# Kernel tuning notes

Measured on AMD Instinct MI355X. Metric: run time of the kernel, lower is better.

Reference implementation:

```python
import jax, jax.numpy as jnp
import numpy as np
from jax import lax

VDECAY, VTH, GRAD_WIN, GRAD_AMP = 0.5, 0.5, 0.5, 1.0

@jax.custom_vjp
def spike(v):
    return (v > VTH).astype(v.dtype)

def _spike_fwd(v):
    return spike(v), v

def _spike_bwd(v, g):
    # rectangular surrogate gradient
    win = (jnp.abs(v - VTH) <= GRAD_WIN).astype(g.dtype)
    return (GRAD_AMP * g * win,)

spike.defvjp(_spike_fwd, _spike_bwd)

def setup_inputs() -> dict:
    key = jax.random.key(0)
    ks = jax.random.split(key, 3)
    B, D_IN, T, H, D_OUT = 256, 700, 250, 1024, 20
    spike_data = (jax.random.uniform(ks[0], (B, D_IN, T)) < 0.1).astype(jnp.float32)
    W_hid = jax.random.normal(ks[1], (H, D_IN), dtype=jnp.float32) * (1.0 / np.sqrt(D_IN))
    W_out = jax.random.normal(ks[2], (D_OUT, H), dtype=jnp.float32) * (1.0 / np.sqrt(H))
    return {
        "spike_data": spike_data,
        "W_hid": W_hid,
        "W_out": W_out,
        "hid_spike0": jnp.zeros((B, H), jnp.float32),
        "hid_volt0": jnp.zeros((B, H), jnp.float32),
        "out_spike0": jnp.zeros((B, D_OUT), jnp.float32),
        "out_volt0": jnp.zeros((B, D_OUT), jnp.float32),
        "batch_size": 256,
        "spike_ts": 250,
    }

def reference(spike_data, W_hid, W_out, hid_spike0, hid_volt0, out_spike0, out_volt0, batch_size, spike_ts):
    # [B, D_in, T] -> [T, B, D_in] for scan over time
    xs = jnp.moveaxis(spike_data.reshape(batch_size, -1, spike_ts), -1, 0)

    def step(carry, s_in):
        hs, hv, os_, ov = carry
        hv = hv * VDECAY * (1.0 - hs) + s_in @ W_hid.T      # leaky integrate, reset on spike
        hs = spike(hv)                                       # hidden spikes
        ov = ov * VDECAY * (1.0 - os_) + hs @ W_out.T
        os_ = spike(ov)
        return (hs, hv, os_, ov), os_

    _, out_spikes = lax.scan(step, (hid_spike0, hid_volt0, out_spike0, out_volt0), xs)
    return jnp.sum(out_spikes, axis=0)  # [B, D_out] spike counts
```

## Files before the change

kernel.cpp:

```cpp
#include <hip/hip_runtime.h>
#include <stdint.h>

#define B      256
#define DIN    700
#define T      250
#define H      1024
#define DOUT   20
#define NW_IN  11
#define NW_INP 12
#define NW_H   16
#define LMAX   160
#define JSENT2 22512

typedef unsigned long long u64;

__global__ void prep_weights(const float* __restrict__ W_hid,
                             const float* __restrict__ W_out,
                             float* __restrict__ Wt,
                             float* __restrict__ WoT) {
    int idx = blockIdx.x * 256 + threadIdx.x;
    if (blockIdx.x < 2800) {
        int d = idx / H;
        int h = idx - d * H;
        Wt[idx] = W_hid[h * DIN + d];
    } else {
        int i = idx - 2800 * 256;
        int h = i / DOUT;
        int o = i - h * DOUT;
        WoT[i] = W_out[o * H + h];
    }
}

__global__ void prep_bits(const float* __restrict__ spk,
                          u64* __restrict__ bits) {
    int b  = blockIdx.x >> 2;
    int wc = blockIdx.x & 3;
    int t  = threadIdx.x;
    if (t >= T) return;
    int w0 = wc * 3;
    int w1 = (wc == 3) ? NW_IN : w0 + 3;
    const float* base = spk + (size_t)b * DIN * T + t;
    for (int w = w0; w < w1; ++w) {
        u64 m = 0;
#pragma unroll
        for (int j = 0; j < 64; ++j) {
            int d = (w << 6) + j;
            if (d < DIN) {
                float x = base[(size_t)d * T];
                m |= (u64)(x > 0.5f) << j;
            }
        }
        bits[((size_t)b * T + t) * NW_INP + w] = m;
    }
}

__global__ void __launch_bounds__(256)
prep_lists2(const u64* __restrict__ bits,
            unsigned short* __restrict__ lists,
            unsigned* __restrict__ nrow) {
    __shared__ unsigned short scr[4][LMAX];

    int wv   = threadIdx.x >> 6;
    int lane = threadIdx.x & 63;
    int row  = blockIdx.x * 4 + wv;

    const u64* wp = bits + (size_t)row * NW_INP;
    u64 mw = (lane < NW_IN) ? wp[lane] : 0ull;

    for (int i = lane; i < LMAX; i += 64) scr[wv][i] = (unsigned short)JSENT2;

    u64 lowmask = (1ull << lane) - 1ull;
    int pos = 0;
    unsigned counts = 0;

#pragma unroll
    for (int p = 0; p < 4; ++p) {
        int jlo = 175 * p, jhi = jlo + 175;
        int n = 0;
        for (int k = jlo >> 6; k <= (jhi - 1) >> 6; ++k) {
            u64 m = __shfl(mw, k);
            int lo = jlo - (k << 6);
            int hi = jhi - (k << 6);
            if (lo > 0)  m &= ~((1ull << lo) - 1ull);
            if (hi < 64) m &= (1ull << hi) - 1ull;
            if ((m >> lane) & 1ull) {
                int q = pos + n + __popcll(m & lowmask);
                int jl = (k << 6) + lane - jlo;
                if (q < LMAX)
                    scr[wv][q] = (unsigned short)(jl * 128 + ((jl & 7) << 4));
            }
            n += __popcll(m);
        }
        int c = (n + 3) >> 2;
        counts |= (unsigned)c << (8 * p);
        pos += c * 4;
    }

    if (lane == 0) nrow[row] = counts;
    __syncthreads();

    const unsigned* s32 = (const unsigned*)scr[wv];
    unsigned* g32 = (unsigned*)(lists + (size_t)row * LMAX);
    g32[lane] = s32[lane];
    if (lane < 16) g32[64 + lane] = s32[64 + lane];
}

__global__ void __launch_bounds__(256)
sort_rows(const unsigned* __restrict__ nrow,
          unsigned char* __restrict__ perm) {
    __shared__ int cnt[8][32];
    __shared__ int off[8][32];
    int b = blockIdx.x, tid = threadIdx.x;
    cnt[tid >> 5][tid & 31] = 0;
    __syncthreads();
    unsigned cc = 0; int half = 0, lt = 0;
    if (tid < T) {
        cc = nrow[b * T + tid];
        half = tid >= 125;
        lt = tid - half * 125;
#pragma unroll
        for (int p = 0; p < 4; ++p) {
            int c = (cc >> (8 * p)) & 0xff; if (c > 31) c = 31;
            atomicAdd(&cnt[p * 2 + half][c], 1);
        }
    }
    __syncthreads();
    if (tid < 8) {
        int s = 0;
        for (int i = 0; i < 32; ++i) { off[tid][i] = s; s += cnt[tid][i]; cnt[tid][i] = 0; }
    }
    __syncthreads();
    if (tid < T) {
#pragma unroll
        for (int p = 0; p < 4; ++p) {
            int c = (cc >> (8 * p)) & 0xff; if (c > 31) c = 31;
            int sidx = p * 2 + half;
            int rank = off[sidx][c] + atomicAdd(&cnt[sidx][c], 1);
            perm[((size_t)b * 8 + sidx) * 128 + rank] = (unsigned char)lt;
        }
    }
}

__global__ void __launch_bounds__(512, 8)
hidden_slice3(const unsigned short* __restrict__ lists,
              const unsigned* __restrict__ nrow,
              const unsigned char* __restrict__ perm,
              const float* __restrict__ Wt,
              const float* __restrict__ hs0,
              const float* __restrict__ hv0,
              u64* __restrict__ hsbits) {
    __shared__ float wlds[176 * 32];
    __shared__ float cur[125 * 32];

    int s    = blockIdx.x;
    int b    = blockIdx.y;
    int tid  = threadIdx.x;
    int wv   = tid >> 6;
    int lane = tid & 63;
    int g    = lane >> 3;
    int li   = lane & 7;
    int lxor = li << 4;
    int l    = lane & 31;

    float keep = 0.0f;
    if (wv == 0) {
        int h = s * 32 + l;
        keep = hv0[b * H + h] * 0.5f * (1.0f - hs0[b * H + h]);
    }
    unsigned* hp = (unsigned*)hsbits;

    for (int th = 0; th < 2; ++th) {
        for (int p = 0; p < 4; ++p) {
            {
                int jr  = tid >> 3;
                int lis = tid & 7;
#pragma unroll
                for (int bj = 0; bj < 192; bj += 64) {
                    int jl = bj + jr;
                    if (jl < 176) {
                        float4 v = make_float4(0.0f, 0.0f, 0.0f, 0.0f);
                        if (jl < 175)
                            v = *(const float4*)(Wt + (size_t)(p * 175 + jl) * H + s * 32 + lis * 4);
                        *(float4*)((char*)wlds + jl * 128 + ((lis ^ (jl & 7)) << 4)) = v;
                    }
                }
            }
            __syncthreads();

            const unsigned char* pm = perm + ((size_t)b * 8 + p * 2 + th) * 128;

#pragma unroll
            for (int sweep = 0; sweep < 2; ++sweep) {
                int rr = sweep * 64 + wv * 8 + g;
                if (rr < 125) {
                    int lr  = pm[rr];
                    int r   = th * 125 + lr;
                    int row = b * T + r;
                    unsigned cc = nrow[row];
                    int c = (cc >> (8 * p)) & 0xff;
                    int offc = 0;
                    if (p > 0) offc += (cc & 0xff);
                    if (p > 1) offc += ((cc >> 8) & 0xff);
                    if (p > 2) offc += ((cc >> 16) & 0xff);
                    const uint2* qp = (const uint2*)(lists + (size_t)row * LMAX + offc * 4);
                    char* cp = (char*)cur + lr * 128 + ((li ^ (lr & 7)) << 4);

                    float a0, a1, a2, a3;
                    if (p == 0) {
                        a0 = a1 = a2 = a3 = 0.0f;
                    } else {
                        float4 cv = *(const float4*)cp;
                        a0 = cv.x; a1 = cv.y; a2 = cv.z; a3 = cv.w;
                    }

                    if (c > 0) {
                        uint2 w2 = qp[0];
                        int ch = 0;
                        for (;;) {
                            uint2 nw = (ch + 1 < c) ? qp[ch + 1] : w2;
                            int e0 = w2.x & 0xffff, e1 = w2.x >> 16;
                            int e2 = w2.y & 0xffff, e3 = w2.y >> 16;
                            float4 v0 = *(const float4*)((char*)wlds + (e0 ^ lxor));
                            float4 v1 = *(const float4*)((char*)wlds + (e1 ^ lxor));
                            float4 v2 = *(const float4*)((char*)wlds + (e2 ^ lxor));
                            float4 v3 = *(const float4*)((char*)wlds + (e3 ^ lxor));
                            a0 += v0.x; a1 += v0.y; a2 += v0.z; a3 += v0.w;
                            a0 += v1.x; a1 += v1.y; a2 += v1.z; a3 += v1.w;
                            a0 += v2.x; a1 += v2.y; a2 += v2.z; a3 += v2.w;
                            a0 += v3.x; a1 += v3.y; a2 += v3.z; a3 += v3.w;
                            ++ch;
                            if (ch >= c) break;
                            w2 = nw;
                        }
                    }
                    float4 o; o.x = a0; o.y = a1; o.z = a2; o.w = a3;
                    *(float4*)cp = o;
                }
            }
            __syncthreads();
        }

        if (wv == 0) {
            for (int lt = 0; lt < 125; ++lt) {
                float cv = *(const float*)((char*)cur + lt * 128 +
                                           (((l >> 2) ^ (lt & 7)) << 4) + (l & 3) * 4);
                float hv = keep + cv;
                bool sp = hv > 0.5f;
                keep = sp ? 0.0f : hv * 0.5f;
                u64 ball = __ballot(sp);
                int t = th * 125 + lt;
                if (lane == 0)
                    hp[(size_t)(b * T + t) * 32 + s] = (unsigned)ball;
            }
        }
        __syncthreads();
    }
}

__global__ void __launch_bounds__(1024)
hidden_fused(const u64* __restrict__ bits,
             const float* __restrict__ Wt,
             const float* __restrict__ hs0,
             const float* __restrict__ hv0,
             u64* __restrict__ hsbits) {
    __shared__ int idx_l[2][256];

    int b = blockIdx.x;
    int h = threadIdx.x;
    int wv   = h >> 6;
    int lane = h & 63;

    float keep = hv0[b * H + h] * 0.5f * (1.0f - hs0[b * H + h]);

    const u64* bb = bits + (size_t)b * T * NW_INP;

    for (int t = 0; t < T; ++t) {
        const u64* wp = bb + (size_t)t * NW_INP;
        u64 w[NW_IN];
#pragma unroll
        for (int k = 0; k < NW_IN; ++k) w[k] = wp[k];

        int base[NW_IN + 1];
        base[0] = 0;
#pragma unroll
        for (int k = 0; k < NW_IN; ++k) base[k + 1] = base[k] + __popcll(w[k]);
        int n = base[NW_IN];

        int buf = t & 1;
        if (wv < NW_IN) {
            u64 m = w[wv];
            if ((m >> lane) & 1ull) {
                int pos = base[wv] + __popcll(m & ((1ull << lane) - 1ull));
                idx_l[buf][pos] = (wv << 6) + lane;
            }
        }
        __syncthreads();

        const int* il = idx_l[buf];
        float cur2 = 0.0f;
        int i = 0;
        for (; i + 8 <= n; i += 8) {
            int j0 = il[i + 0], j1 = il[i + 1], j2 = il[i + 2], j3 = il[i + 3];
            int j4 = il[i + 4], j5 = il[i + 5], j6 = il[i + 6], j7 = il[i + 7];
            float v0 = Wt[(size_t)j0 * H + h];
            float v1 = Wt[(size_t)j1 * H + h];
            float v2 = Wt[(size_t)j2 * H + h];
            float v3 = Wt[(size_t)j3 * H + h];
            float v4 = Wt[(size_t)j4 * H + h];
            float v5 = Wt[(size_t)j5 * H + h];
            float v6 = Wt[(size_t)j6 * H + h];
            float v7 = Wt[(size_t)j7 * H + h];
            cur2 += v0; cur2 += v1; cur2 += v2; cur2 += v3;
            cur2 += v4; cur2 += v5; cur2 += v6; cur2 += v7;
        }
        for (; i < n; ++i) cur2 += Wt[(size_t)il[i] * H + h];

        float hv = keep + cur2;
        bool sp = hv > 0.5f;
        keep = sp ? 0.0f : hv * 0.5f;
        u64 ball = __ballot(sp);
        if (lane == 0)
            hsbits[((size_t)b * T + t) * NW_H + wv] = ball;
    }
}

__global__ void __launch_bounds__(256)
out_currents(const u64* __restrict__ hsbits,
             const float* __restrict__ WoT,
             float* __restrict__ Iout) {
    __shared__ int lidx[4][2][256];

    int wv   = threadIdx.x >> 6;
    int lane = threadIdx.x & 63;
    int row  = blockIdx.x * 4 + wv;

    const u64* wp = hsbits + (size_t)row * NW_H;

    float acc = 0.0f;
#pragma unroll
    for (int g = 0; g < 4; ++g) {
        u64 w[4];
#pragma unroll
        for (int k = 0; k < 4; ++k) w[k] = wp[g * 4 + k];

        int base[5];
        base[0] = 0;
#pragma unroll
        for (int k = 0; k < 4; ++k) base[k + 1] = base[k] + __popcll(w[k]);
        int n = base[4];

        int buf = g & 1;
#pragma unroll
        for (int k = 0; k < 4; ++k) {
            u64 m = w[k];
            if ((m >> lane) & 1ull) {
                int pos = base[k] + __popcll(m & ((1ull << lane) - 1ull));
                lidx[wv][buf][pos] = ((g * 4 + k) << 6) + lane;
            }
        }
        __syncthreads();

        const int* il = lidx[wv][buf];
        int i = 0;
        for (; i + 4 <= n; i += 4) {
            int j0 = il[i + 0], j1 = il[i + 1], j2 = il[i + 2], j3 = il[i + 3];
            if (lane < DOUT) {
                float v0 = WoT[(size_t)j0 * DOUT + lane];
                float v1 = WoT[(size_t)j1 * DOUT + lane];
                float v2 = WoT[(size_t)j2 * DOUT + lane];
                float v3 = WoT[(size_t)j3 * DOUT + lane];
                acc += v0; acc += v1; acc += v2; acc += v3;
            }
        }
        for (; i < n; ++i) {
            if (lane < DOUT) acc += WoT[(size_t)il[i] * DOUT + lane];
        }
    }
    if (lane < DOUT) Iout[(size_t)row * DOUT + lane] = acc;
}

__global__ void __launch_bounds__(256)
out_scan(const float* __restrict__ Iout,
         const float* __restrict__ os0,
         const float* __restrict__ ov0,
         float* __restrict__ outp) {
    __shared__ float pan[T * DOUT];

    int b   = blockIdx.x;
    int tid = threadIdx.x;

    const float* src = Iout + (size_t)b * T * DOUT;
#pragma unroll
    for (int k = 0; k < 20; ++k) {
        int i = k * 256 + tid;
        if (i < T * DOUT) pan[i] = src[i];
    }
    __syncthreads();

    if (tid < DOUT) {
        int o = tid;
        int idx = b * DOUT + o;
        float ov = ov0[idx];
        float os = os0[idx];
        float keep = ov * 0.5f * (1.0f - os);
        float cnt = 0.0f;
#pragma unroll 5
        for (int t = 0; t < T; ++t) {
            float v = keep + pan[t * DOUT + o];
            float sp = (v > 0.5f) ? 1.0f : 0.0f;
            cnt += sp;
            keep = v * 0.5f * (1.0f - sp);
        }
        outp[idx] = cnt;
    }
}

extern "C" void kernel_launch(void* const* d_in, const int* in_sizes, int n_in,
                              void* d_out, int out_size, void* d_ws, size_t ws_size,
                              hipStream_t stream) {
    const float* spike = (const float*)d_in[0];
    const float* W_hid = (const float*)d_in[1];
    const float* W_out = (const float*)d_in[2];
    const float* hs0   = (const float*)d_in[3];
    const float* hv0   = (const float*)d_in[4];
    const float* os0   = (const float*)d_in[5];
    const float* ov0   = (const float*)d_in[6];
    float* outp = (float*)d_out;

    char* ws = (char*)d_ws;
    float*          Wt     = (float*)(ws);
    float*          WoT    = (float*)(ws + 2867200);
    u64*            bits   = (u64*)  (ws + 2949120);
    u64*            hsbits = (u64*)  (ws + 9093120);
    float*          Iout   = (float*)(ws + 17285120);
    unsigned short* lists  = (unsigned short*)(ws + 22405120);
    unsigned*       nrow   = (unsigned*)(ws + 42885120);
    unsigned char*  perm   = (unsigned char*)(ws + 43141120);
    const size_t need = 43403264;

    prep_weights<<<2880, 256, 0, stream>>>(W_hid, W_out, Wt, WoT);
    prep_bits<<<1024, 256, 0, stream>>>(spike, bits);

    if (ws_size >= need) {
        prep_lists2<<<16000, 256, 0, stream>>>(bits, lists, nrow);
        sort_rows<<<B, 256, 0, stream>>>(nrow, perm);
        hidden_slice3<<<dim3(32, 256), 512, 0, stream>>>(lists, nrow, perm, Wt, hs0, hv0, hsbits);
    } else {
        hidden_fused<<<B, 1024, 0, stream>>>(bits, Wt, hs0, hv0, hsbits);
    }

    out_currents<<<16000, 256, 0, stream>>>(hsbits, WoT, Iout);
    out_scan<<<B, 256, 0, stream>>>(Iout, os0, ov0, outp);
}
```

Baseline: 988.0 us.

## Stage W_out^T in LDS and pack three rows per wave in out_currents

The output-current kernel now copies the whole transposed output weight matrix (80 KB) into shared memory once per block. Each wave then handles three (batch, time) rows at once, using 60 of its 64 lanes, and walks the set bits of the hidden spike mask with ctz instead of building index lists in LDS. This removes the per-row list compaction, the barriers and the global gathers, and uses more lanes per wave. In exchange each block must fill 80 KB of LDS, which limits occupancy. Lanes in a wave loop different numbers of times, so they diverge.

```diff
diff --git a/kernel.cpp b/kernel.cpp
--- a/kernel.cpp
+++ b/kernel.cpp
@@ -324,59 +324,46 @@
     }
 }
 
-__global__ void __launch_bounds__(256)
-out_currents(const u64* __restrict__ hsbits,
-             const float* __restrict__ WoT,
-             float* __restrict__ Iout) {
-    __shared__ int lidx[4][2][256];
-
-    int wv   = threadIdx.x >> 6;
-    int lane = threadIdx.x & 63;
-    int row  = blockIdx.x * 4 + wv;
+__global__ void __launch_bounds__(512)
+out_currents2(const u64* __restrict__ hsbits,
+              const float* __restrict__ WoT,
+              float* __restrict__ Iout) {
+    __shared__ float wot[H * DOUT];
+
+    int tid = threadIdx.x;
+    {
+        const float4* src = (const float4*)WoT;
+        float4* dst = (float4*)wot;
+#pragma unroll
+        for (int k = 0; k < 10; ++k)
+            dst[k * 512 + tid] = src[k * 512 + tid];
+    }
+    __syncthreads();
+
+    int wv   = tid >> 6;
+    int lane = tid & 63;
+    int sub  = lane / 20;
+    int o    = lane - sub * 20;
+    int row  = blockIdx.x * 24 + wv * 3 + sub;
+    if (sub >= 3 || row >= B * T) return;
 
     const u64* wp = hsbits + (size_t)row * NW_H;
+    u64 w[NW_H];
+#pragma unroll
+    for (int k = 0; k < NW_H; ++k) w[k] = wp[k];
 
     float acc = 0.0f;
 #pragma unroll
-    for (int g = 0; g < 4; ++g) {
-        u64 w[4];
-#pragma unroll
-        for (int k = 0; k < 4; ++k) w[k] = wp[g * 4 + k];
-
-        int base[5];
-        base[0] = 0;
-#pragma unroll
-        for (int k = 0; k < 4; ++k) base[k + 1] = base[k] + __popcll(w[k]);
-        int n = base[4];
-
-        int buf = g & 1;
-#pragma unroll
-        for (int k = 0; k < 4; ++k) {
-            u64 m = w[k];
-            if ((m >> lane) & 1ull) {
-                int pos = base[k] + __popcll(m & ((1ull << lane) - 1ull));
-                lidx[wv][buf][pos] = ((g * 4 + k) << 6) + lane;
-            }
-        }
-        __syncthreads();
-
-        const int* il = lidx[wv][buf];
-        int i = 0;
-        for (; i + 4 <= n; i += 4) {
-            int j0 = il[i + 0], j1 = il[i + 1], j2 = il[i + 2], j3 = il[i + 3];
-            if (lane < DOUT) {
-                float v0 = WoT[(size_t)j0 * DOUT + lane];
-                float v1 = WoT[(size_t)j1 * DOUT + lane];
-                float v2 = WoT[(size_t)j2 * DOUT + lane];
-                float v3 = WoT[(size_t)j3 * DOUT + lane];
-                acc += v0; acc += v1; acc += v2; acc += v3;
-            }
-        }
-        for (; i < n; ++i) {
-            if (lane < DOUT) acc += WoT[(size_t)il[i] * DOUT + lane];
-        }
-    }
-    if (lane < DOUT) Iout[(size_t)row * DOUT + lane] = acc;
+    for (int k = 0; k < NW_H; ++k) {
+        u64 m = w[k];
+        const float* base = wot + k * 64 * DOUT + o;
+        while (m) {
+            int h0 = __builtin_ctzll(m);
+            m &= m - 1;
+            acc += base[h0 * DOUT];
+        }
+    }
+    Iout[(size_t)row * DOUT + o] = acc;
 }
 
 __global__ void __launch_bounds__(256)
@@ -449,6 +436,6 @@
         hidden_fused<<<B, 1024, 0, stream>>>(bits, Wt, hs0, hv0, hsbits);
     }
 
-    out_currents<<<16000, 256, 0, stream>>>(hsbits, WoT, Iout);
+    out_currents2<<<2667, 512, 0, stream>>>(hsbits, WoT, Iout);
     out_scan<<<B, 256, 0, stream>>>(Iout, os0, ov0, outp);
 }
```

Result: faster. 965.4 us (-2.3%).
